# Performance work log

Hardware: AMD Instinct MI355X
Metric: run time of the kernel (lower is better)

Reference implementation:

```python
import jax, jax.numpy as jnp
import numpy as np

WEIGHT = 1.0

def setup_inputs() -> dict:
    key = jax.random.key(0)
    k1, k2 = jax.random.split(key)
    shape = (64, 17, 256, 256)  # [batch, joints, H, W]
    output = jax.random.normal(k1, shape, dtype=jnp.float32)
    target = jax.random.normal(k2, shape, dtype=jnp.float32)
    return {"output": output, "target": target}

def reference(output, target):
    # Original: loss = sum_{b,j} mean_{H,W}((out[b,j]-tgt[b,j])^2) / batches * weight
    batches = output.shape[0]
    diff = output - target
    per_bj_mse = jnp.mean(diff * diff, axis=(2, 3))  # [B, J]
    loss = jnp.sum(per_bj_mse) / batches * WEIGHT
    return loss
```

## Files before the change

kernel.cpp:

```cpp
#include <hip/hip_runtime.h>


#define THREADS 256
#define PER_THREAD 32

using f4 = __attribute__((ext_vector_type(4))) float;

__global__ __launch_bounds__(THREADS) void mse_partial_kernel(
    const f4* __restrict__ a4, const f4* __restrict__ b4,
    float* __restrict__ partial) {
    int base = blockIdx.x * (THREADS * PER_THREAD) + threadIdx.x;

    float acc = 0.0f;
    #pragma unroll 8
    for (int k = 0; k < PER_THREAD; ++k) {
        f4 x = __builtin_nontemporal_load(&a4[base + k * THREADS]);
        f4 y = __builtin_nontemporal_load(&b4[base + k * THREADS]);
        f4 d = x - y;
        acc = fmaf(d.x, d.x, acc);
        acc = fmaf(d.y, d.y, acc);
        acc = fmaf(d.z, d.z, acc);
        acc = fmaf(d.w, d.w, acc);
    }

    #pragma unroll
    for (int off = 32; off >= 1; off >>= 1)
        acc += __shfl_down(acc, off, 64);

    __shared__ float wsum[THREADS / 64];
    int lane = threadIdx.x & 63;
    int wid = threadIdx.x >> 6;
    if (lane == 0) wsum[wid] = acc;
    __syncthreads();

    if (threadIdx.x == 0) {
        float s = 0.0f;
        #pragma unroll
        for (int w = 0; w < THREADS / 64; ++w) s += wsum[w];
        partial[blockIdx.x] = s;
    }
}

__global__ __launch_bounds__(THREADS) void mse_final_kernel(
    const float* __restrict__ partial, int nb,
    const float* __restrict__ a, const float* __restrict__ b,
    int tail_start, int n,
    float* __restrict__ out, float scale) {
    float acc = 0.0f;
    for (int i = threadIdx.x; i < nb; i += THREADS) acc += partial[i];
    for (int i = tail_start + threadIdx.x; i < n; i += THREADS) {
        float d = a[i] - b[i];
        acc = fmaf(d, d, acc);
    }

    #pragma unroll
    for (int off = 32; off >= 1; off >>= 1)
        acc += __shfl_down(acc, off, 64);

    __shared__ float wsum[THREADS / 64];
    int lane = threadIdx.x & 63;
    int wid = threadIdx.x >> 6;
    if (lane == 0) wsum[wid] = acc;
    __syncthreads();

    if (threadIdx.x == 0) {
        float s = 0.0f;
        #pragma unroll
        for (int w = 0; w < THREADS / 64; ++w) s += wsum[w];
        out[0] = s * scale;
    }
}

extern "C" void kernel_launch(void* const* d_in, const int* in_sizes, int n_in,
                              void* d_out, int out_size, void* d_ws, size_t ws_size,
                              hipStream_t stream) {
    const float* a = (const float*)d_in[0];
    const float* b = (const float*)d_in[1];
    float* out = (float*)d_out;
    float* partial = (float*)d_ws;

    int n = in_sizes[0];
    int n4 = n >> 2;
    int per_block = THREADS * PER_THREAD;
    int blocks = n4 / per_block;
    int tail_start = blocks * per_block * 4;

    const float scale = 1.0f / (256.0f * 256.0f * 64.0f);

    mse_partial_kernel<<<blocks, THREADS, 0, stream>>>(
        (const f4*)a, (const f4*)b, partial);
    mse_final_kernel<<<1, THREADS, 0, stream>>>(
        partial, blocks, a, b, tail_start, n, out, scale);
}
```

Measured before the change: 89.56 us.

## Fuse final reduction into main kernel via last-block atomic counter

Merges the two-kernel reduction into one kernel: each block writes its partial sum, bumps an atomic counter, and the last block to finish sums the partials and the tail. The grid is fixed at 2048 blocks with a runtime per-thread count, where the old grid was sized by a constant per-thread count of 32. The aim is to remove the second kernel launch and the gap between kernels. A memset launch is added to reset the counter, and the per-thread loop count is now a runtime value, which may change how the loop unrolls.

After: 192.9 us. 115% more time.

```diff
diff --git a/kernel.cpp b/kernel.cpp
--- a/kernel.cpp
+++ b/kernel.cpp
@@ -2,18 +2,39 @@
 
 
 #define THREADS 256
-#define PER_THREAD 32
 
 using f4 = __attribute__((ext_vector_type(4))) float;
 
-__global__ __launch_bounds__(THREADS) void mse_partial_kernel(
+__device__ __forceinline__ float block_reduce(float acc, float* wsum) {
+    #pragma unroll
+    for (int off = 32; off >= 1; off >>= 1)
+        acc += __shfl_down(acc, off, 64);
+    int lane = threadIdx.x & 63;
+    int wid = threadIdx.x >> 6;
+    if (lane == 0) wsum[wid] = acc;
+    __syncthreads();
+    float s = 0.0f;
+    if (threadIdx.x == 0) {
+        #pragma unroll
+        for (int w = 0; w < THREADS / 64; ++w) s += wsum[w];
+    }
+    return s;
+}
+
+__global__ __launch_bounds__(THREADS) void mse_kernel(
     const f4* __restrict__ a4, const f4* __restrict__ b4,
-    float* __restrict__ partial) {
-    int base = blockIdx.x * (THREADS * PER_THREAD) + threadIdx.x;
+    const float* __restrict__ a, const float* __restrict__ b,
+    float* __restrict__ partial, unsigned int* __restrict__ counter,
+    int per_thread, int tail_start, int n,
+    float* __restrict__ out, float scale) {
+    __shared__ float wsum[THREADS / 64];
+    __shared__ int is_last;
+
+    int base = blockIdx.x * (THREADS * per_thread) + threadIdx.x;
 
     float acc = 0.0f;
     #pragma unroll 8
-    for (int k = 0; k < PER_THREAD; ++k) {
+    for (int k = 0; k < per_thread; ++k) {
         f4 x = __builtin_nontemporal_load(&a4[base + k * THREADS]);
         f4 y = __builtin_nontemporal_load(&b4[base + k * THREADS]);
         f4 d = x - y;
@@ -23,51 +44,28 @@
         acc = fmaf(d.w, d.w, acc);
     }
 
-    #pragma unroll
-    for (int off = 32; off >= 1; off >>= 1)
-        acc += __shfl_down(acc, off, 64);
+    float s = block_reduce(acc, wsum);
 
-    __shared__ float wsum[THREADS / 64];
-    int lane = threadIdx.x & 63;
-    int wid = threadIdx.x >> 6;
-    if (lane == 0) wsum[wid] = acc;
+    if (threadIdx.x == 0) {
+        partial[blockIdx.x] = s;
+        __threadfence();
+        unsigned int old = atomicAdd(counter, 1u);
+        is_last = (old == gridDim.x - 1) ? 1 : 0;
+    }
     __syncthreads();
 
-    if (threadIdx.x == 0) {
-        float s = 0.0f;
-        #pragma unroll
-        for (int w = 0; w < THREADS / 64; ++w) s += wsum[w];
-        partial[blockIdx.x] = s;
-    }
-}
-
-__global__ __launch_bounds__(THREADS) void mse_final_kernel(
-    const float* __restrict__ partial, int nb,
-    const float* __restrict__ a, const float* __restrict__ b,
-    int tail_start, int n,
-    float* __restrict__ out, float scale) {
-    float acc = 0.0f;
-    for (int i = threadIdx.x; i < nb; i += THREADS) acc += partial[i];
-    for (int i = tail_start + threadIdx.x; i < n; i += THREADS) {
-        float d = a[i] - b[i];
-        acc = fmaf(d, d, acc);
-    }
-
-    #pragma unroll
-    for (int off = 32; off >= 1; off >>= 1)
-        acc += __shfl_down(acc, off, 64);
-
-    __shared__ float wsum[THREADS / 64];
-    int lane = threadIdx.x & 63;
-    int wid = threadIdx.x >> 6;
-    if (lane == 0) wsum[wid] = acc;
-    __syncthreads();
-
-    if (threadIdx.x == 0) {
-        float s = 0.0f;
-        #pragma unroll
-        for (int w = 0; w < THREADS / 64; ++w) s += wsum[w];
-        out[0] = s * scale;
+    if (is_last) {
+        __threadfence();
+        float facc = 0.0f;
+        for (int i = threadIdx.x; i < (int)gridDim.x; i += THREADS)
+            facc += partial[i];
+        for (int i = tail_start + threadIdx.x; i < n; i += THREADS) {
+            float d = a[i] - b[i];
+            facc = fmaf(d, d, facc);
+        }
+        __syncthreads();
+        float fs = block_reduce(facc, wsum);
+        if (threadIdx.x == 0) out[0] = fs * scale;
     }
 }
 
@@ -77,18 +75,20 @@
     const float* a = (const float*)d_in[0];
     const float* b = (const float*)d_in[1];
     float* out = (float*)d_out;
+
     float* partial = (float*)d_ws;
+    unsigned int* counter = (unsigned int*)((char*)d_ws + (64 * 1024));
 
     int n = in_sizes[0];
     int n4 = n >> 2;
-    int per_block = THREADS * PER_THREAD;
-    int blocks = n4 / per_block;
-    int tail_start = blocks * per_block * 4;
+    const int blocks = 2048;
+    int per_thread = n4 / (blocks * THREADS);
+    int tail_start = blocks * THREADS * per_thread * 4;
 
     const float scale = 1.0f / (256.0f * 256.0f * 64.0f);
 
-    mse_partial_kernel<<<blocks, THREADS, 0, stream>>>(
-        (const f4*)a, (const f4*)b, partial);
-    mse_final_kernel<<<1, THREADS, 0, stream>>>(
-        partial, blocks, a, b, tail_start, n, out, scale);
+    hipMemsetAsync(counter, 0, sizeof(unsigned int), stream);
+    mse_kernel<<<blocks, THREADS, 0, stream>>>(
+        (const f4*)a, (const f4*)b, a, b, partial, counter,
+        per_thread, tail_start, n, out, scale);
 }
```
